# Kernel optimization log

Hardware: AMD Instinct MI355X
Metric: run time of the kernel (lower is better)

The kernel has to match this reference:

```python
import jax, jax.numpy as jnp
import numpy as np

U, I, D, L, NNZ = 8000, 16000, 64, 2, 768000
N = U + I


def setup_inputs() -> dict:
    key = jax.random.key(0)
    ks = jax.random.split(key, 10)
    return {
        "user_indices": jnp.arange(U, dtype=jnp.int64) if jax.config.jax_enable_x64 else jnp.arange(U, dtype=jnp.int32),
        "item_indices": jnp.arange(I, dtype=jnp.int32),
        "adj_rows": jax.random.randint(ks[0], (NNZ,), 0, N, dtype=jnp.int32),
        "adj_cols": jax.random.randint(ks[1], (NNZ,), 0, N, dtype=jnp.int32),
        "adj_vals": jax.random.uniform(ks[2], (NNZ,), dtype=jnp.float32),
        "user_emb": 0.1 * jax.random.normal(ks[3], (U, D), dtype=jnp.float32),
        "item_emb": 0.1 * jax.random.normal(ks[4], (I, D), dtype=jnp.float32),
        "gc_W": 0.05 * jax.random.normal(ks[5], (L, D, D), dtype=jnp.float32),
        "gc_b": jnp.zeros((L, D), dtype=jnp.float32),
        "bi_W": 0.05 * jax.random.normal(ks[6], (L, D, D), dtype=jnp.float32),
        "bi_b": jnp.zeros((L, D), dtype=jnp.float32),
    }


def reference(user_indices, item_indices, adj_rows, adj_cols, adj_vals,
              user_emb, item_emb, gc_W, gc_b, bi_W, bi_b):
    # embedding lookups + concat -> ego embeddings [N, D]
    ego = jnp.concatenate([user_emb[user_indices], item_emb[item_indices]], axis=0)
    n_nodes = ego.shape[0]
    all_embeddings = [ego]
    n_layers = gc_W.shape[0]
    for l in range(n_layers):
        # sparse.mm(adj, ego): gather neighbor rows, weight, scatter-add to rows
        side = jax.ops.segment_sum(adj_vals[:, None] * ego[adj_cols], adj_rows,
                                   num_segments=n_nodes)  # [N, D]
        sum_emb = jax.nn.leaky_relu(side @ gc_W[l].T + gc_b[l], negative_slope=0.01)
        bi_emb = jax.nn.leaky_relu((ego * side) @ bi_W[l].T + bi_b[l], negative_slope=0.01)
        ego = sum_emb + bi_emb
        all_embeddings.append(ego)
    all_emb = jnp.concatenate(all_embeddings, axis=1)  # [N, D*(L+1)]
    n_users = user_indices.shape[0]
    u_g = all_emb[:n_users]
    i_g = all_emb[n_users:]
    scores = u_g @ i_g.T  # [U, I]
    return jax.nn.log_softmax(scores, axis=1)
```

## Files before the change

### kernel.cpp

```cpp
#include <hip/hip_runtime.h>
#include <hip/hip_bf16.h>
#include <math.h>

#define NU   8000
#define NI   16000
#define NN   24000
#define DD   64
#define NL   2
#define NNZS 768000
#define KD   192
#define NCH  25
#define ACHUNK 640
#define CTILES 5
#define RBLK 63
#define CBLK 125
#define SCH  24

typedef __attribute__((ext_vector_type(8))) short  short8;
typedef __attribute__((ext_vector_type(4))) float  f32x4;

__device__ __forceinline__ unsigned short f2bf(float x) {
    union { float f; unsigned int u; } v; v.f = x;
    unsigned int r = v.u + 0x7fff + ((v.u >> 16) & 1);
    return (unsigned short)(r >> 16);
}
__device__ __forceinline__ float bf2f(unsigned short u) {
    union { unsigned int u; float f; } v; v.u = ((unsigned int)u) << 16;
    return v.f;
}

__device__ __forceinline__ int bslot(int nf, int kt, int g, int r16) {
    return ((((kt * 8 + nf) * 4 + g) * 16) + r16) ^ ((g + 4 * kt) & 7);
}

__global__ void k_concat(const int* __restrict__ uidx, const int* __restrict__ iidx,
                         const float* __restrict__ ue, const float* __restrict__ ie,
                         const float* __restrict__ gcW, const float* __restrict__ biW,
                         unsigned short* __restrict__ allemb,
                         unsigned short* __restrict__ wbf, int* __restrict__ cnt) {
    int t = blockIdx.x * blockDim.x + threadIdx.x;
    if (t < NN) cnt[t] = 0;
    if (t < NL * DD * DD) {
        wbf[t] = f2bf(gcW[t]);
        wbf[NL * DD * DD + t] = f2bf(biW[t]);
    }
    if (t >= NN * DD) return;
    int n = t >> 6, d = t & 63;
    float v = (n < NU) ? ue[uidx[n] * DD + d] : ie[iidx[n - NU] * DD + d];
    allemb[(size_t)n * KD + d] = f2bf(v);
}

__global__ void k_hist(const int* __restrict__ rows, int* __restrict__ cnt) {
    int e = blockIdx.x * blockDim.x + threadIdx.x;
    if (e < NNZS) atomicAdd(&cnt[rows[e]], 1);
}

__global__ __launch_bounds__(1024) void k_scan1(const int* __restrict__ cnt,
                                                int* __restrict__ rp, int* __restrict__ btot) {
    __shared__ int wsum[16];
    int tid = threadIdx.x, lane = tid & 63, wid = tid >> 6;
    int i = blockIdx.x * 1024 + tid;
    int v = (i < NN) ? cnt[i] : 0;
    int x = v;
#pragma unroll
    for (int off = 1; off < 64; off <<= 1) {
        int t = __shfl_up(x, off, 64);
        if (lane >= off) x += t;
    }
    if (lane == 63) wsum[wid] = x;
    __syncthreads();
    if (tid < 16) {
        int y = wsum[tid];
#pragma unroll
        for (int off = 1; off < 16; off <<= 1) {
            int t = __shfl_up(y, off, 64);
            if (tid >= off) y += t;
        }
        wsum[tid] = y;
    }
    __syncthreads();
    int incl = x + (wid ? wsum[wid - 1] : 0);
    if (i < NN) rp[i + 1] = incl;
    if (tid == 0) btot[blockIdx.x] = wsum[15];
}

__global__ void k_scan2(const int* __restrict__ btot, int* __restrict__ boff) {
    int tid = threadIdx.x;
    int v = (tid < SCH) ? btot[tid] : 0;
    int x = v;
#pragma unroll
    for (int off = 1; off < 32; off <<= 1) {
        int t = __shfl_up(x, off, 64);
        if (tid >= off) x += t;
    }
    if (tid < SCH) boff[tid] = x - v;
}

__global__ __launch_bounds__(1024) void k_scan3(const int* __restrict__ cnt,
                                                const int* __restrict__ boff,
                                                int* __restrict__ rp, int* __restrict__ wp) {
    int i = blockIdx.x * 1024 + threadIdx.x;
    if (i == 0) rp[0] = 0;
    if (i >= NN) return;
    int g = rp[i + 1] + boff[blockIdx.x];
    rp[i + 1] = g;
    wp[i] = g - cnt[i];
}

__global__ void k_scatter(const int* __restrict__ rows, const int* __restrict__ cols,
                          const float* __restrict__ vals, int* __restrict__ wp,
                          int2* __restrict__ edat) {
    int e = blockIdx.x * blockDim.x + threadIdx.x;
    if (e >= NNZS) return;
    int r = rows[e];
    int pos = atomicAdd(&wp[r], 1);
    edat[pos] = make_int2(cols[e], __float_as_int(vals[e]));
}

__global__ __launch_bounds__(256) void k_layer(const int* __restrict__ rp, const int2* __restrict__ edat,
                        unsigned short* __restrict__ allemb, int l,
                        const unsigned short* __restrict__ wg_bf,
                        const unsigned short* __restrict__ wb_bf,
                        const float* __restrict__ gcb, const float* __restrict__ bib) {
    __shared__ float sideS[4][16][66];
    int tid = threadIdx.x, lane = tid & 63, wave = tid >> 6;
    int n0 = blockIdx.x * 64 + wave * 16;
    const unsigned short* feat = allemb + l * DD;

    for (int k = 0; k < 16; ++k) {
        int n = n0 + k;
        int e0 = rp[n], e1 = rp[n + 1];
        float acc = 0.f;
        int e = e0;
        for (; e + 8 <= e1; e += 8) {
            int2 d[8];
#pragma unroll
            for (int j = 0; j < 8; ++j) d[j] = edat[e + j];
#pragma unroll
            for (int j = 0; j < 8; ++j)
                acc = fmaf(__int_as_float(d[j].y), bf2f(feat[(size_t)d[j].x * KD + lane]), acc);
        }
        for (; e < e1; ++e) {
            int2 d = edat[e];
            acc = fmaf(__int_as_float(d.y), bf2f(feat[(size_t)d.x * KD + lane]), acc);
        }
        sideS[wave][k][lane] = acc;
    }

    int nrow = lane & 15, kofs = (lane >> 4) * 8, g = lane >> 4;
    short8 bg[4][2], bb[4][2];
#pragma unroll
    for (int nf = 0; nf < 4; ++nf)
#pragma unroll
        for (int kt = 0; kt < 2; ++kt) {
            bg[nf][kt] = *(const short8*)(wg_bf + (nf * 16 + nrow) * DD + kt * 32 + kofs);
            bb[nf][kt] = *(const short8*)(wb_bf + (nf * 16 + nrow) * DD + kt * 32 + kofs);
        }

    short8 a1[2], a2[2];
    const unsigned short* ep = feat + (size_t)(n0 + nrow) * KD;
#pragma unroll
    for (int kt = 0; kt < 2; ++kt) {
        int o = kt * 32 + kofs;
#pragma unroll
        for (int j = 0; j < 8; ++j) {
            float s = sideS[wave][nrow][o + j];
            float e = bf2f(ep[o + j]);
            a1[kt][j] = (short)f2bf(s);
            a2[kt][j] = (short)f2bf(e * s);
        }
    }

    f32x4 acc1[4], acc2[4];
#pragma unroll
    for (int nf = 0; nf < 4; ++nf) { acc1[nf] = (f32x4){0,0,0,0}; acc2[nf] = (f32x4){0,0,0,0}; }
#pragma unroll
    for (int nf = 0; nf < 4; ++nf)
#pragma unroll
        for (int kt = 0; kt < 2; ++kt) {
            acc1[nf] = __builtin_amdgcn_mfma_f32_16x16x32_bf16(a1[kt], bg[nf][kt], acc1[nf], 0, 0, 0);
            acc2[nf] = __builtin_amdgcn_mfma_f32_16x16x32_bf16(a2[kt], bb[nf][kt], acc2[nf], 0, 0, 0);
        }

#pragma unroll
    for (int nf = 0; nf < 4; ++nf) {
        int o = nf * 16 + nrow;
        float b1 = gcb[o], b2 = bib[o];
#pragma unroll
        for (int r = 0; r < 4; ++r) {
            int node = n0 + g * 4 + r;
            float v1 = acc1[nf][r] + b1;
            float v2 = acc2[nf][r] + b2;
            v1 = v1 > 0.f ? v1 : 0.01f * v1;
            v2 = v2 > 0.f ? v2 : 0.01f * v2;
            allemb[(size_t)node * KD + (l + 1) * DD + o] = f2bf(v1 + v2);
        }
    }
}

__global__ __launch_bounds__(256) void k_lse_part(const unsigned short* __restrict__ allemb,
                                                  float* __restrict__ pm, float* __restrict__ ps) {
    __shared__ short8 Bs[3072];
    int id = blockIdx.x;
    int rowblk = id % RBLK;
    int chunk  = id / RBLK;
    int tid = threadIdx.x;
    int lane = tid & 63;
    int wave = tid >> 6;
    int r0 = rowblk * 128 + wave * 32;
    int c0 = chunk * ACHUNK;
    const unsigned short* A = allemb;
    const unsigned short* B = allemb + (size_t)NU * KD;
    int kofs = (lane >> 4) * 8;
    int g = lane >> 4;

    short8 a[2][6];
#pragma unroll
    for (int mi = 0; mi < 2; ++mi) {
        int ar = r0 + mi * 16 + (lane & 15);
        if (ar >= NU) ar = NU - 1;
#pragma unroll
        for (int kt = 0; kt < 6; ++kt)
            a[mi][kt] = *(const short8*)(A + (size_t)ar * KD + kt * 32 + kofs);
    }

    float m[2][4], s[2][4];
#pragma unroll
    for (int mi = 0; mi < 2; ++mi)
#pragma unroll
        for (int r = 0; r < 4; ++r) { m[mi][r] = -INFINITY; s[mi][r] = 0.f; }

    for (int t = 0; t < CTILES; ++t) {
        const unsigned short* Bt = B + (size_t)(c0 + t * 128) * KD;
        __syncthreads();
#pragma unroll
        for (int i = 0; i < 12; ++i) {
            int mm = i * 256 + tid;
            int r = mm / 24, c = mm - r * 24;
            int kt = c >> 2, gg = c & 3;
            Bs[bslot(r >> 4, kt, gg, r & 15)] = *(const short8*)(Bt + (size_t)r * KD + c * 8);
        }
        __syncthreads();

        f32x4 acc[2][8];
#pragma unroll
        for (int mi = 0; mi < 2; ++mi)
#pragma unroll
            for (int nf = 0; nf < 8; ++nf) acc[mi][nf] = (f32x4){0.f, 0.f, 0.f, 0.f};
#pragma unroll
        for (int nf = 0; nf < 8; ++nf)
#pragma unroll
            for (int kt = 0; kt < 6; ++kt) {
                short8 b = Bs[bslot(nf, kt, g, lane & 15)];
                acc[0][nf] = __builtin_amdgcn_mfma_f32_16x16x32_bf16(a[0][kt], b, acc[0][nf], 0, 0, 0);
                acc[1][nf] = __builtin_amdgcn_mfma_f32_16x16x32_bf16(a[1][kt], b, acc[1][nf], 0, 0, 0);
            }
#pragma unroll
        for (int mi = 0; mi < 2; ++mi)
#pragma unroll
            for (int r = 0; r < 4; ++r) {
                float lm = acc[mi][0][r];
#pragma unroll
                for (int nf = 1; nf < 8; ++nf) lm = fmaxf(lm, acc[mi][nf][r]);
                float nm = fmaxf(m[mi][r], lm);
                float p = 0.f;
#pragma unroll
                for (int nf = 0; nf < 8; ++nf) p += __expf(acc[mi][nf][r] - nm);
                s[mi][r] = s[mi][r] * __expf(m[mi][r] - nm) + p;
                m[mi][r] = nm;
            }
    }
#pragma unroll
    for (int mi = 0; mi < 2; ++mi)
#pragma unroll
        for (int r = 0; r < 4; ++r) {
            float mm = m[mi][r], ss = s[mi][r];
#pragma unroll
            for (int off = 1; off < 16; off <<= 1) {
                float om = __shfl_xor(mm, off, 64);
                float os = __shfl_xor(ss, off, 64);
                float nm = fmaxf(mm, om);
                ss = ss * __expf(mm - nm) + os * __expf(om - nm);
                mm = nm;
            }
            m[mi][r] = mm; s[mi][r] = ss;
        }
    if ((lane & 15) == 0) {
#pragma unroll
        for (int mi = 0; mi < 2; ++mi)
#pragma unroll
            for (int r = 0; r < 4; ++r) {
                int row = r0 + mi * 16 + g * 4 + r;
                if (row < NU) {
                    pm[chunk * NU + row] = m[mi][r];
                    ps[chunk * NU + row] = s[mi][r];
                }
            }
    }
}

__global__ void k_lse_comb(const float* __restrict__ pm, const float* __restrict__ ps,
                           float* __restrict__ lse) {
    int r = blockIdx.x * blockDim.x + threadIdx.x;
    if (r >= NU) return;
    float m = -INFINITY;
    for (int c = 0; c < NCH; ++c) m = fmaxf(m, pm[c * NU + r]);
    float s = 0.f;
    for (int c = 0; c < NCH; ++c) s += ps[c * NU + r] * __expf(pm[c * NU + r] - m);
    lse[r] = m + __logf(s);
}

__global__ __launch_bounds__(256) void k_out(const unsigned short* __restrict__ allemb,
                                             const float* __restrict__ lse, float* __restrict__ out) {
    __shared__ short8 Bs[3072];
    int id = blockIdx.x;
    int rowblk = id / CBLK;
    int colblk = id % CBLK;
    int tid = threadIdx.x;
    int lane = tid & 63;
    int wave = tid >> 6;
    int r0 = rowblk * 128 + wave * 32;
    int c0 = colblk * 128;
    const unsigned short* A = allemb;
    const unsigned short* B = allemb + (size_t)NU * KD;
    int kofs = (lane >> 4) * 8;
    int g = lane >> 4;

    const unsigned short* Bt = B + (size_t)c0 * KD;
#pragma unroll
    for (int i = 0; i < 12; ++i) {
        int mm = i * 256 + tid;
        int r = mm / 24, c = mm - r * 24;
        int kt = c >> 2, gg = c & 3;
        Bs[bslot(r >> 4, kt, gg, r & 15)] = *(const short8*)(Bt + (size_t)r * KD + c * 8);
    }

    short8 a[2][6];
#pragma unroll
    for (int mi = 0; mi < 2; ++mi) {
        int ar = r0 + mi * 16 + (lane & 15);
        if (ar >= NU) ar = NU - 1;
#pragma unroll
        for (int kt = 0; kt < 6; ++kt)
            a[mi][kt] = *(const short8*)(A + (size_t)ar * KD + kt * 32 + kofs);
    }
    float l4[2][4];
#pragma unroll
    for (int mi = 0; mi < 2; ++mi)
#pragma unroll
        for (int r = 0; r < 4; ++r) {
            int row = r0 + mi * 16 + g * 4 + r;
            l4[mi][r] = lse[row >= NU ? NU - 1 : row];
        }
    __syncthreads();

    f32x4 acc[2][8];
#pragma unroll
    for (int mi = 0; mi < 2; ++mi)
#pragma unroll
        for (int nf = 0; nf < 8; ++nf) acc[mi][nf] = (f32x4){0.f, 0.f, 0.f, 0.f};
#pragma unroll
    for (int nf = 0; nf < 8; ++nf)
#pragma unroll
        for (int kt = 0; kt < 6; ++kt) {
            short8 b = Bs[bslot(nf, kt, g, lane & 15)];
            acc[0][nf] = __builtin_amdgcn_mfma_f32_16x16x32_bf16(a[0][kt], b, acc[0][nf], 0, 0, 0);
            acc[1][nf] = __builtin_amdgcn_mfma_f32_16x16x32_bf16(a[1][kt], b, acc[1][nf], 0, 0, 0);
        }
    __syncthreads();

    float* tilef = (float*)Bs;
    float* tW = tilef + wave * 16 * 132;
#pragma unroll
    for (int mi = 0; mi < 2; ++mi) {
        int rowbase = r0 + mi * 16;
#pragma unroll
        for (int nf = 0; nf < 8; ++nf)
#pragma unroll
            for (int r = 0; r < 4; ++r)
                tW[(g * 4 + r) * 132 + nf * 16 + (lane & 15)] = acc[mi][nf][r] - l4[mi][r];
#pragma unroll
        for (int it = 0; it < 8; ++it) {
            int idx = it * 64 + lane;
            int rr = idx >> 5;
            int cc = (idx & 31) * 4;
            int row = rowbase + rr;
            if (row < NU) {
                f32x4 v = *(const f32x4*)&tW[rr * 132 + cc];
                __builtin_nontemporal_store(v, (f32x4*)&out[(size_t)row * NI + c0 + cc]);
            }
        }
    }
}

extern "C" void kernel_launch(void* const* d_in, const int* in_sizes, int n_in,
                              void* d_out, int out_size, void* d_ws, size_t ws_size,
                              hipStream_t stream) {
    const int*   uidx = (const int*)d_in[0];
    const int*   iidx = (const int*)d_in[1];
    const int*   arow = (const int*)d_in[2];
    const int*   acol = (const int*)d_in[3];
    const float* aval = (const float*)d_in[4];
    const float* ue   = (const float*)d_in[5];
    const float* ie   = (const float*)d_in[6];
    const float* gcW  = (const float*)d_in[7];
    const float* gcb  = (const float*)d_in[8];
    const float* biW  = (const float*)d_in[9];
    const float* bib  = (const float*)d_in[10];
    float* out = (float*)d_out;

    char* w = (char*)d_ws;
    unsigned short* allemb = (unsigned short*)w;  w += (size_t)NN * KD * sizeof(unsigned short);
    float* pm  = (float*)w;                       w += (size_t)NCH * NU * sizeof(float);
    float* ps  = (float*)w;                       w += (size_t)NCH * NU * sizeof(float);
    float* lse = (float*)w;                       w += (size_t)NU * sizeof(float);
    unsigned short* wbf = (unsigned short*)w;     w += (size_t)2 * NL * DD * DD * sizeof(unsigned short);
    int* cnt   = (int*)w;                         w += (size_t)NN * sizeof(int);
    int* rp    = (int*)w;                         w += (size_t)(NN + 4) * sizeof(int);
    int* wp    = (int*)w;                         w += (size_t)NN * sizeof(int);
    int* btot  = (int*)w;                         w += 32 * sizeof(int);
    int* boff  = (int*)w;                         w += 32 * sizeof(int);
    int2* edat = (int2*)w;                        w += (size_t)NNZS * sizeof(int2);

    unsigned short* wg_bf = wbf;
    unsigned short* wb_bf = wbf + NL * DD * DD;

    k_concat<<<(NN * DD + 255) / 256, 256, 0, stream>>>(uidx, iidx, ue, ie, gcW, biW,
                                                        allemb, wbf, cnt);

    k_hist<<<(NNZS + 255) / 256, 256, 0, stream>>>(arow, cnt);
    k_scan1<<<SCH, 1024, 0, stream>>>(cnt, rp, btot);
    k_scan2<<<1, 64, 0, stream>>>(btot, boff);
    k_scan3<<<SCH, 1024, 0, stream>>>(cnt, boff, rp, wp);
    k_scatter<<<(NNZS + 255) / 256, 256, 0, stream>>>(arow, acol, aval, wp, edat);

    for (int l = 0; l < NL; ++l)
        k_layer<<<NN / 64, 256, 0, stream>>>(rp, edat, allemb, l,
                                             wg_bf + l * DD * DD, wb_bf + l * DD * DD,
                                             gcb + l * DD, bib + l * DD);

    k_lse_part<<<RBLK * NCH, 256, 0, stream>>>(allemb, pm, ps);
    k_lse_comb<<<(NU + 255) / 256, 256, 0, stream>>>(pm, ps, lse);
    k_out<<<RBLK * CBLK, 256, 0, stream>>>(allemb, lse, out);
}
```

Before: 546.3 us.

## Split fused GNN layer into separate CSR SpMM and dense MFMA kernels

Splits the fused per-layer kernel into two. The first is a CSR SpMM kernel that assigns one wave per row and writes the aggregated side embeddings to a global fp32 buffer. The second is a dense kernel that reads that buffer and does the MFMA transforms. The aim is to spread the sparse aggregation across many more waves, so it no longer runs 16 rows serially per wave, and to decouple its load imbalance from the dense stage. In exchange it adds a global write and read of a 24000x64 float buffer and an extra kernel launch per layer.

```diff
diff --git a/kernel.cpp b/kernel.cpp
--- a/kernel.cpp
+++ b/kernel.cpp
@@ -117,37 +117,43 @@
     edat[pos] = make_int2(cols[e], __float_as_int(vals[e]));
 }
 
-__global__ __launch_bounds__(256) void k_layer(const int* __restrict__ rp, const int2* __restrict__ edat,
+__global__ void k_spmm_csr(const int* __restrict__ rp, const int2* __restrict__ edat,
+                           const unsigned short* __restrict__ feat, float* __restrict__ side) {
+    int lane = threadIdx.x & 63;
+    int wave = (blockIdx.x * blockDim.x + threadIdx.x) >> 6;
+    int nw   = (gridDim.x * blockDim.x) >> 6;
+    for (int r = wave; r < NN; r += nw) {
+        int e0 = rp[r], e1 = rp[r + 1];
+        float acc = 0.f;
+        int e = e0;
+        for (; e + 8 <= e1; e += 8) {
+            int2 d[8];
+#pragma unroll
+            for (int j = 0; j < 8; ++j) d[j] = edat[e + j];
+#pragma unroll
+            for (int j = 0; j < 8; ++j)
+                acc = fmaf(__int_as_float(d[j].y), bf2f(feat[(size_t)d[j].x * KD + lane]), acc);
+        }
+        for (; e < e1; ++e) {
+            int2 d = edat[e];
+            acc = fmaf(__int_as_float(d.y), bf2f(feat[(size_t)d.x * KD + lane]), acc);
+        }
+        side[(size_t)r * DD + lane] = acc;
+    }
+}
+
+__global__ __launch_bounds__(256) void k_dense(const float* __restrict__ side,
                         unsigned short* __restrict__ allemb, int l,
                         const unsigned short* __restrict__ wg_bf,
                         const unsigned short* __restrict__ wb_bf,
                         const float* __restrict__ gcb, const float* __restrict__ bib) {
-    __shared__ float sideS[4][16][66];
-    int tid = threadIdx.x, lane = tid & 63, wave = tid >> 6;
-    int n0 = blockIdx.x * 64 + wave * 16;
+    int lane = threadIdx.x & 63;
+    int wave = threadIdx.x >> 6;
+    int n0 = (blockIdx.x * 4 + wave) * 16;
+    int nrow = lane & 15;
+    int kofs = (lane >> 4) * 8;
     const unsigned short* feat = allemb + l * DD;
 
-    for (int k = 0; k < 16; ++k) {
-        int n = n0 + k;
-        int e0 = rp[n], e1 = rp[n + 1];
-        float acc = 0.f;
-        int e = e0;
-        for (; e + 8 <= e1; e += 8) {
-            int2 d[8];
-#pragma unroll
-            for (int j = 0; j < 8; ++j) d[j] = edat[e + j];
-#pragma unroll
-            for (int j = 0; j < 8; ++j)
-                acc = fmaf(__int_as_float(d[j].y), bf2f(feat[(size_t)d[j].x * KD + lane]), acc);
-        }
-        for (; e < e1; ++e) {
-            int2 d = edat[e];
-            acc = fmaf(__int_as_float(d.y), bf2f(feat[(size_t)d.x * KD + lane]), acc);
-        }
-        sideS[wave][k][lane] = acc;
-    }
-
-    int nrow = lane & 15, kofs = (lane >> 4) * 8, g = lane >> 4;
     short8 bg[4][2], bb[4][2];
 #pragma unroll
     for (int nf = 0; nf < 4; ++nf)
@@ -158,13 +164,14 @@
         }
 
     short8 a1[2], a2[2];
+    const float* sp = side + (size_t)(n0 + nrow) * DD;
     const unsigned short* ep = feat + (size_t)(n0 + nrow) * KD;
 #pragma unroll
     for (int kt = 0; kt < 2; ++kt) {
         int o = kt * 32 + kofs;
 #pragma unroll
         for (int j = 0; j < 8; ++j) {
-            float s = sideS[wave][nrow][o + j];
+            float s = sp[o + j];
             float e = bf2f(ep[o + j]);
             a1[kt][j] = (short)f2bf(s);
             a2[kt][j] = (short)f2bf(e * s);
@@ -182,6 +189,7 @@
             acc2[nf] = __builtin_amdgcn_mfma_f32_16x16x32_bf16(a2[kt], bb[nf][kt], acc2[nf], 0, 0, 0);
         }
 
+    int g = lane >> 4;
 #pragma unroll
     for (int nf = 0; nf < 4; ++nf) {
         int o = nf * 16 + nrow;
@@ -411,6 +419,7 @@
 
     char* w = (char*)d_ws;
     unsigned short* allemb = (unsigned short*)w;  w += (size_t)NN * KD * sizeof(unsigned short);
+    float* side = (float*)w;                      w += (size_t)NN * DD * sizeof(float);
     float* pm  = (float*)w;                       w += (size_t)NCH * NU * sizeof(float);
     float* ps  = (float*)w;                       w += (size_t)NCH * NU * sizeof(float);
     float* lse = (float*)w;                       w += (size_t)NU * sizeof(float);
@@ -434,10 +443,12 @@
     k_scan3<<<SCH, 1024, 0, stream>>>(cnt, boff, rp, wp);
     k_scatter<<<(NNZS + 255) / 256, 256, 0, stream>>>(arow, acol, aval, wp, edat);
 
-    for (int l = 0; l < NL; ++l)
-        k_layer<<<NN / 64, 256, 0, stream>>>(rp, edat, allemb, l,
+    for (int l = 0; l < NL; ++l) {
+        k_spmm_csr<<<3000, 256, 0, stream>>>(rp, edat, allemb + l * DD, side);
+        k_dense<<<NN / 64, 256, 0, stream>>>(side, allemb, l,
                                              wg_bf + l * DD * DD, wb_bf + l * DD * DD,
                                              gcb + l * DD, bib + l * DD);
+    }
 
     k_lse_part<<<RBLK * NCH, 256, 0, stream>>>(allemb, pm, ps);
     k_lse_comb<<<(NU + 255) / 256, 256, 0, stream>>>(pm, ps, lse);
```

Result: faster. 485.6 us (-11.1%).
